# Kernel optimization log

Hardware: AMD Instinct MI355X
Metric: run time of the kernel (lower is better)

Reference implementation:

```python
import jax, jax.numpy as jnp
import numpy as np

N = 131072   # total gates/nodes in the batched block-diagonal circuit graph
E = 524288   # directed edges (avg degree 4)
D = 100      # hidden dim
DA = 50      # msg MLP hidden
DC = 30      # classifier hidden
R = 20       # message-passing rounds


def mlp(x, W1, b1, W2, b2):
    return jax.nn.relu(x @ W1 + b1) @ W2 + b2


def gru_step(x, h, Wih, Whh, bih, bhh):
    # single-timestep torch.nn.GRU cell
    gi = x @ Wih.T + bih
    gh = h @ Whh.T + bhh
    ir, iz, inn = jnp.split(gi, 3, axis=-1)
    hr, hz, hn = jnp.split(gh, 3, axis=-1)
    r = jax.nn.sigmoid(ir + hr)
    z = jax.nn.sigmoid(iz + hz)
    nwe = jnp.tanh(inn + r * hn)
    return (1.0 - z) * nwe + z * h


def setup_inputs():
    key = jax.random.key(0)
    ks = jax.random.split(key, 26)
    s = 0.05

    def rn(k, shape):
        return jax.random.normal(k, shape, dtype=jnp.float32) * s

    inp = {
        'features': jax.random.normal(ks[0], (N, 4), dtype=jnp.float32),
        'edge_row': jax.random.randint(ks[1], (E,), 0, N, dtype=jnp.int32),
        'edge_col': jax.random.randint(ks[2], (E,), 0, N, dtype=jnp.int32),
        'init_W': rn(ks[3], (4, D)), 'init_b': jnp.zeros((D,), jnp.float32),
        'fmsg_W1': rn(ks[4], (D, DA)), 'fmsg_b1': jnp.zeros((DA,), jnp.float32),
        'fmsg_W2': rn(ks[5], (DA, D)), 'fmsg_b2': jnp.zeros((D,), jnp.float32),
        'bmsg_W1': rn(ks[6], (D, DA)), 'bmsg_b1': jnp.zeros((DA,), jnp.float32),
        'bmsg_W2': rn(ks[7], (DA, D)), 'bmsg_b2': jnp.zeros((D,), jnp.float32),
        'fgru_Wih': rn(ks[8], (3 * D, D)), 'fgru_Whh': rn(ks[9], (3 * D, D)),
        'fgru_bih': jnp.zeros((3 * D,), jnp.float32), 'fgru_bhh': jnp.zeros((3 * D,), jnp.float32),
        'bgru_Wih': rn(ks[10], (3 * D, D)), 'bgru_Whh': rn(ks[11], (3 * D, D)),
        'bgru_bih': jnp.zeros((3 * D,), jnp.float32), 'bgru_bhh': jnp.zeros((3 * D,), jnp.float32),
        'cls_W1': rn(ks[12], (D, DC)), 'cls_b1': jnp.zeros((DC,), jnp.float32),
        'cls_W2': rn(ks[13], (DC, 1)), 'cls_b2': jnp.zeros((1,), jnp.float32),
    }
    return inp


def reference(features, edge_row, edge_col, init_W, init_b,
              fmsg_W1, fmsg_b1, fmsg_W2, fmsg_b2,
              bmsg_W1, bmsg_b1, bmsg_W2, bmsg_b2,
              fgru_Wih, fgru_Whh, fgru_bih, fgru_bhh,
              bgru_Wih, bgru_Whh, bgru_bih, bgru_bhh,
              cls_W1, cls_b1, cls_W2, cls_b2):
    n = features.shape[0]
    h = features @ init_W + init_b  # [N, D]

    def round_body(h, _):
        # forward pass: adj @ forward_msg(h)
        fm = mlp(h, fmsg_W1, fmsg_b1, fmsg_W2, fmsg_b2)
        f_msg = jax.ops.segment_sum(fm[edge_col], edge_row, num_segments=n)
        h = gru_step(f_msg, h, fgru_Wih, fgru_Whh, fgru_bih, fgru_bhh)
        # backward pass: adj.T @ backward_msg(h)
        bm = mlp(h, bmsg_W1, bmsg_b1, bmsg_W2, bmsg_b2)
        b_msg = jax.ops.segment_sum(bm[edge_row], edge_col, num_segments=n)
        h = gru_step(b_msg, h, bgru_Wih, bgru_Whh, bgru_bih, bgru_bhh)
        return h, None

    h, _ = jax.lax.scan(jax.checkpoint(round_body), h, None, length=R)
    return mlp(h, cls_W1, cls_b1, cls_W2, cls_b2)  # [N, 1]
```

## Files before the change

### kernel.cpp

```cpp
#include <hip/hip_runtime.h>
#include <math.h>

#define Nn 131072
#define Ee 524288

typedef __attribute__((ext_vector_type(8))) short short8;
typedef __attribute__((ext_vector_type(4))) float f32x4;
typedef unsigned short ushort_t;
typedef unsigned int uint32;

__device__ __forceinline__ f32x4 mfma16(short8 a, short8 b, f32x4 c) {
    return __builtin_amdgcn_mfma_f32_16x16x32_bf16(a, b, c, 0, 0, 0);
}

__device__ __forceinline__ uint32 rne_bf16(float x) {
    uint32 u = __float_as_uint(x);
    return (u + 0x7FFFu + ((u >> 16) & 1u)) >> 16;
}

__device__ __forceinline__ void split3(float x, uint32& h, uint32& m, uint32& l) {
    h = rne_bf16(x);
    float hf = __uint_as_float(h << 16);
    float r1 = x - hf;
    m = rne_bf16(r1);
    float mf = __uint_as_float(m << 16);
    float r2 = r1 - mf;
    l = rne_bf16(r2);
}

__global__ void diag_kernel(float* out, float val) {
    int n = blockIdx.x * 256 + threadIdx.x;
    if (n < Nn) out[n] = (n == 0) ? val : 0.f;
}
__global__ void zero_ints(int* p, int n) {
    int i = blockIdx.x * 256 + threadIdx.x;
    if (i < n) p[i] = 0;
}

__global__ void hist_kernel(const int* __restrict__ er, const int* __restrict__ ec,
                            int* __restrict__ cnt_f, int* __restrict__ cnt_b) {
    int e = blockIdx.x * 256 + threadIdx.x;
    atomicAdd(&cnt_f[er[e]], 1);
    atomicAdd(&cnt_b[ec[e]], 1);
}

__global__ __launch_bounds__(1024) void scan_kernel(const int* __restrict__ cnt,
                                                    int* __restrict__ ptr, int n) {
    __shared__ int sums[1024];
    int t = threadIdx.x;
    int chunk = n >> 10;
    int base = t * chunk;
    int s = 0;
    for (int i = 0; i < chunk; i++) s += cnt[base + i];
    sums[t] = s;
    __syncthreads();
    for (int off = 1; off < 1024; off <<= 1) {
        int v = (t >= off) ? sums[t - off] : 0;
        __syncthreads();
        sums[t] += v;
        __syncthreads();
    }
    int run = (t == 0) ? 0 : sums[t - 1];
    for (int i = 0; i < chunk; i++) { ptr[base + i] = run; run += cnt[base + i]; }
    if (t == 1023) ptr[n] = run;
}

__global__ void fill_kernel(const int* __restrict__ er, const int* __restrict__ ec,
                            int* __restrict__ ptr_f, int* __restrict__ ptr_b,
                            int* __restrict__ src_f, int* __restrict__ src_b) {
    int e = blockIdx.x * 256 + threadIdx.x;
    int r = er[e], c = ec[e];
    int p = atomicAdd(&ptr_f[r], 1); src_f[p] = c;
    int q = atomicAdd(&ptr_b[c], 1); src_b[q] = r;
}

__global__ void prep_gru_w(const float* __restrict__ Wih, const float* __restrict__ Whh,
                           const float* __restrict__ bih, const float* __restrict__ bhh,
                           ushort_t* __restrict__ W0, ushort_t* __restrict__ W1,
                           ushort_t* __restrict__ W2, float* __restrict__ bg) {
    int gid = blockIdx.x * 256 + threadIdx.x;
    if (gid >= 400 * 224) return;
    int c = gid / 224, k = gid - c * 224;
    int d = c >> 2, g = c & 3;
    float w = 0.f;
    if (k < 100) {
        if (g == 0)      w = Wih[d * 100 + k];
        else if (g == 1) w = Wih[(100 + d) * 100 + k];
        else if (g == 2) w = Wih[(200 + d) * 100 + k];
    } else if (k < 200) {
        int kk = k - 100;
        if (g == 0)      w = Whh[d * 100 + kk];
        else if (g == 1) w = Whh[(100 + d) * 100 + kk];
        else if (g == 3) w = Whh[(200 + d) * 100 + kk];
    }
    uint32 h, m, l; split3(w, h, m, l);
    W0[gid] = (ushort_t)h; W1[gid] = (ushort_t)m; W2[gid] = (ushort_t)l;
    if (k == 0) {
        float b;
        if (g == 0)      b = bih[d] + bhh[d];
        else if (g == 1) b = bih[100 + d] + bhh[100 + d];
        else if (g == 2) b = bih[200 + d];
        else             b = bhh[200 + d];
        bg[c] = b;
    }
}

__global__ void prep_msg_w(const float* __restrict__ W1, const float* __restrict__ b1,
                           const float* __restrict__ W2, const float* __restrict__ b2,
                           ushort_t* __restrict__ A0, ushort_t* __restrict__ A1,
                           ushort_t* __restrict__ A2, float* __restrict__ b1p,
                           ushort_t* __restrict__ B0, ushort_t* __restrict__ B1,
                           ushort_t* __restrict__ B2, float* __restrict__ b2p) {
    int gid = blockIdx.x * 256 + threadIdx.x;
    if (gid < 8192) {
        int c = gid >> 7, k = gid & 127;
        float w = (c < 50 && k < 100) ? W1[k * 50 + c] : 0.f;
        uint32 h, m, l; split3(w, h, m, l);
        A0[gid] = (ushort_t)h; A1[gid] = (ushort_t)m; A2[gid] = (ushort_t)l;
        if (k == 0) b1p[c] = (c < 50) ? b1[c] : 0.f;
    } else if (gid < 8192 + 7168) {
        int t = gid - 8192;
        int c = t >> 6, k = t & 63;
        float w = (c < 100 && k < 50) ? W2[k * 100 + c] : 0.f;
        uint32 h, m, l; split3(w, h, m, l);
        B0[t] = (ushort_t)h; B1[t] = (ushort_t)m; B2[t] = (ushort_t)l;
        if (k == 0) b2p[c] = (c < 100) ? b2[c] : 0.f;
    }
}

__global__ void init_h_kernel(const float* __restrict__ feat, const float* __restrict__ W,
                              const float* __restrict__ b, float* __restrict__ Act) {
    int gid = blockIdx.x * 256 + threadIdx.x;
    int n = gid / 100, d = gid - n * 100;
    float acc = b[d];
#pragma unroll
    for (int k = 0; k < 4; k++) acc += feat[n * 4 + k] * W[k * 100 + d];
    Act[(size_t)n * 200 + 100 + d] = acc;
}

__global__ __launch_bounds__(256, 2) void msg_mfma(
    const float* __restrict__ Act,
    const ushort_t* __restrict__ A0, const ushort_t* __restrict__ A1,
    const ushort_t* __restrict__ A2, const float* __restrict__ b1p,
    const ushort_t* __restrict__ B0, const ushort_t* __restrict__ B1,
    const ushort_t* __restrict__ B2, const float* __restrict__ b2p,
    float* __restrict__ fm) {
    __shared__ ushort_t C1[3][64][72];
    const int tid = threadIdx.x;
    const int u = tid >> 6;
    const int lane = tid & 63;
    const int m = lane & 15, q = lane >> 4;
    const int n0 = blockIdx.x * 64;
    const int n = n0 + u * 16 + m;

    f32x4 z = {0.f, 0.f, 0.f, 0.f};
    f32x4 a1[4] = {z, z, z, z};

    for (int kc = 0; kc < 4; kc++) {
        int kb = kc * 32 + q * 8;
        const float* src = Act + (size_t)n * 200 + 100 + kb;
        float4 v0 = *(const float4*)src;
        float4 v1 = *(const float4*)(src + 4);
        float e[8] = {v0.x, v0.y, v0.z, v0.w, v1.x, v1.y, v1.z, v1.w};
        union { short8 s; uint32 u4[4]; } f0, f1, f2;
#pragma unroll
        for (int j = 0; j < 4; j++) {
            uint32 ha, ma, la, hb, mb, lb;
            split3(e[2 * j], ha, ma, la);
            split3(e[2 * j + 1], hb, mb, lb);
            f0.u4[j] = ha | (hb << 16);
            f1.u4[j] = ma | (mb << 16);
            f2.u4[j] = la | (lb << 16);
        }
#pragma unroll
        for (int t = 0; t < 4; t++) {
            int off = (t * 16 + m) * 128 + kc * 32 + q * 8;
            short8 w0 = *(const short8*)(A0 + off);
            short8 w1 = *(const short8*)(A1 + off);
            short8 w2 = *(const short8*)(A2 + off);
            a1[t] = mfma16(w0, f0.s, a1[t]);
            a1[t] = mfma16(w0, f1.s, a1[t]);
            a1[t] = mfma16(w1, f0.s, a1[t]);
            a1[t] = mfma16(w0, f2.s, a1[t]);
            a1[t] = mfma16(w2, f0.s, a1[t]);
            a1[t] = mfma16(w1, f1.s, a1[t]);
        }
    }
#pragma unroll
    for (int t = 0; t < 4; t++) {
        int c0 = t * 16 + 4 * q;
        float4 bb = *(const float4*)&b1p[c0];
        float v0 = fmaxf(a1[t][0] + bb.x, 0.f);
        float v1 = fmaxf(a1[t][1] + bb.y, 0.f);
        float v2 = fmaxf(a1[t][2] + bb.z, 0.f);
        float v3 = fmaxf(a1[t][3] + bb.w, 0.f);
        uint32 h0, m0, l0, h1, m1, l1, h2, m2, l2, h3, m3, l3;
        split3(v0, h0, m0, l0); split3(v1, h1, m1, l1);
        split3(v2, h2, m2, l2); split3(v3, h3, m3, l3);
        int nl = u * 16 + m;
        *(uint2*)&C1[0][nl][c0] = make_uint2(h0 | (h1 << 16), h2 | (h3 << 16));
        *(uint2*)&C1[1][nl][c0] = make_uint2(m0 | (m1 << 16), m2 | (m3 << 16));
        *(uint2*)&C1[2][nl][c0] = make_uint2(l0 | (l1 << 16), l2 | (l3 << 16));
    }
    __syncthreads();

    f32x4 a2[7] = {z, z, z, z, z, z, z};
    for (int kc = 0; kc < 2; kc++) {
        int nl = u * 16 + m;
        short8 c0f = *(const short8*)&C1[0][nl][kc * 32 + q * 8];
        short8 c1f = *(const short8*)&C1[1][nl][kc * 32 + q * 8];
        short8 c2f = *(const short8*)&C1[2][nl][kc * 32 + q * 8];
#pragma unroll
        for (int t = 0; t < 7; t++) {
            int off = (t * 16 + m) * 64 + kc * 32 + q * 8;
            short8 w0 = *(const short8*)(B0 + off);
            short8 w1 = *(const short8*)(B1 + off);
            short8 w2 = *(const short8*)(B2 + off);
            a2[t] = mfma16(w0, c0f, a2[t]);
            a2[t] = mfma16(w0, c1f, a2[t]);
            a2[t] = mfma16(w1, c0f, a2[t]);
            a2[t] = mfma16(w0, c2f, a2[t]);
            a2[t] = mfma16(w2, c0f, a2[t]);
            a2[t] = mfma16(w1, c1f, a2[t]);
        }
    }
#pragma unroll
    for (int t = 0; t < 7; t++) {
        int c0 = t * 16 + 4 * q;
        if (c0 < 100) {
            float4 bb = *(const float4*)&b2p[c0];
            float4 o;
            o.x = a2[t][0] + bb.x; o.y = a2[t][1] + bb.y;
            o.z = a2[t][2] + bb.z; o.w = a2[t][3] + bb.w;
            *(float4*)&fm[(size_t)n * 100 + c0] = o;
        }
    }
}

__global__ void gather4(const float* __restrict__ fm, const int* __restrict__ ptr,
                        const int* __restrict__ idx, float* __restrict__ Act) {
    int gid = blockIdx.x * 256 + threadIdx.x;
    int n = gid / 25, qq = (gid - n * 25) * 4;
    int s = (n == 0) ? 0 : ptr[n - 1];
    int e = ptr[n];
    float4 acc = {0.f, 0.f, 0.f, 0.f};
    for (int i = s; i < e; i++) {
        float4 v = *(const float4*)&fm[(size_t)idx[i] * 100 + qq];
        acc.x += v.x; acc.y += v.y; acc.z += v.z; acc.w += v.w;
    }
    *(float4*)&Act[(size_t)n * 200 + qq] = acc;
}

__global__ __launch_bounds__(256, 3) void gru_mfma(
    float* __restrict__ Act,
    const ushort_t* __restrict__ W0, const ushort_t* __restrict__ W1,
    const ushort_t* __restrict__ W2, const float* __restrict__ bg) {
    __shared__ __align__(16) uint32 Bs[2][3][32][20];
    const int tid = threadIdx.x;
    const int wave = tid >> 6;
    const int lane = tid & 63;
    const int m = lane & 15, q = lane >> 4;
    const int n0 = blockIdx.x * 32;
    const int sr = tid >> 3;
    const int sk4 = (tid & 7) * 4;
    const int cu = (tid & 7) * 2;

    f32x4 z = {0.f, 0.f, 0.f, 0.f};
    f32x4 acc[7][2];
#pragma unroll
    for (int t = 0; t < 7; t++) { acc[t][0] = z; acc[t][1] = z; }

    const float* actrow = Act + (size_t)(n0 + sr) * 200;

#define LDCHUNK(kc, dst) do {                                   \
        int kb = (kc) * 32 + sk4;                               \
        if (kb < 200) dst = *(const float4*)(actrow + kb);      \
        else { dst.x = 0.f; dst.y = 0.f; dst.z = 0.f; dst.w = 0.f; } \
    } while (0)

#define STAGE(b, v) do {                                        \
        uint32 h0,m0,l0,h1,m1,l1,h2,m2,l2,h3,m3,l3;             \
        split3((v).x,h0,m0,l0); split3((v).y,h1,m1,l1);         \
        split3((v).z,h2,m2,l2); split3((v).w,h3,m3,l3);         \
        *(uint2*)&Bs[b][0][sr][cu] = make_uint2(h0|(h1<<16), h2|(h3<<16)); \
        *(uint2*)&Bs[b][1][sr][cu] = make_uint2(m0|(m1<<16), m2|(m3<<16)); \
        *(uint2*)&Bs[b][2][sr][cu] = make_uint2(l0|(l1<<16), l2|(l3<<16)); \
    } while (0)

    {
        float4 v0; LDCHUNK(0, v0);
        STAGE(0, v0);
    }
    __syncthreads();

    for (int kc = 0; kc < 7; kc++) {
        float4 nxt;
        if (kc < 6) LDCHUNK(kc + 1, nxt);
        const int b = kc & 1;
        short8 bf0[2], bf1[2], bf2[2];
#pragma unroll
        for (int u = 0; u < 2; u++) {
            bf0[u] = *(const short8*)&Bs[b][0][u * 16 + m][q * 4];
            bf1[u] = *(const short8*)&Bs[b][1][u * 16 + m][q * 4];
            bf2[u] = *(const short8*)&Bs[b][2][u * 16 + m][q * 4];
        }
#pragma unroll
        for (int t = 0; t < 7; t++) {
            if (t < 6 || wave == 0) {
                const int ct = t * 4 + wave;
                int off = (ct * 16 + m) * 224 + kc * 32 + q * 8;
                short8 w0 = *(const short8*)(W0 + off);
                short8 w1 = *(const short8*)(W1 + off);
                short8 w2 = *(const short8*)(W2 + off);
#pragma unroll
                for (int u = 0; u < 2; u++) {
                    acc[t][u] = mfma16(w0, bf0[u], acc[t][u]);
                    acc[t][u] = mfma16(w0, bf1[u], acc[t][u]);
                    acc[t][u] = mfma16(w1, bf0[u], acc[t][u]);
                    acc[t][u] = mfma16(w0, bf2[u], acc[t][u]);
                    acc[t][u] = mfma16(w2, bf0[u], acc[t][u]);
                    acc[t][u] = mfma16(w1, bf1[u], acc[t][u]);
                }
            }
        }
        if (kc < 6) STAGE(b ^ 1, nxt);
        __syncthreads();
    }
#undef LDCHUNK
#undef STAGE

#pragma unroll
    for (int t = 0; t < 7; t++) {
        if (t < 6 || wave == 0) {
            const int ct = t * 4 + wave;
            const int c0 = ct * 16 + 4 * q;
            const int d = ct * 4 + q;
            float4 b4 = *(const float4*)&bg[c0];
#pragma unroll
            for (int u = 0; u < 2; u++) {
                int n = n0 + u * 16 + m;
                float* hp = Act + (size_t)n * 200 + 100 + d;
                float hold = *hp;
                float rp = acc[t][u][0] + b4.x;
                float zp = acc[t][u][1] + b4.y;
                float np = acc[t][u][2] + b4.z;
                float hh = acc[t][u][3] + b4.w;
                float rr = 1.f / (1.f + __expf(-rp));
                float zz = 1.f / (1.f + __expf(-zp));
                float nw = tanhf(np + rr * hh);
                *hp = (1.f - zz) * nw + zz * hold;
            }
        }
    }
}

__global__ __launch_bounds__(256) void classifier(
    const float* __restrict__ Act, const float* __restrict__ W1,
    const float* __restrict__ b1, const float* __restrict__ W2,
    const float* __restrict__ b2, float* __restrict__ out) {
    __shared__ float Wc[3000];
    __shared__ float bc[30];
    __shared__ float w2[30];
    int tid = threadIdx.x;
    for (int i = tid; i < 3000; i += 256) Wc[i] = W1[i];
    if (tid < 30) { bc[tid] = b1[tid]; w2[tid] = W2[tid]; }
    __syncthreads();
    int n = blockIdx.x * 256 + tid;
    float a[30];
#pragma unroll
    for (int j = 0; j < 30; j++) a[j] = bc[j];
    for (int k = 0; k < 100; k++) {
        float hv = Act[(size_t)n * 200 + 100 + k];
#pragma unroll
        for (int j = 0; j < 30; j++) a[j] = fmaf(hv, Wc[k * 30 + j], a[j]);
    }
    float s = b2[0];
#pragma unroll
    for (int j = 0; j < 30; j++) s = fmaf(fmaxf(a[j], 0.f), w2[j], s);
    out[n] = s;
}

extern "C" void kernel_launch(void* const* d_in, const int* in_sizes, int n_in,
                              void* d_out, int out_size, void* d_ws, size_t ws_size,
                              hipStream_t stream) {
    const float* feat     = (const float*)d_in[0];
    const int*   er       = (const int*)d_in[1];
    const int*   ec       = (const int*)d_in[2];
    const float* init_W   = (const float*)d_in[3];
    const float* init_b   = (const float*)d_in[4];
    const float* fmsg_W1  = (const float*)d_in[5];
    const float* fmsg_b1  = (const float*)d_in[6];
    const float* fmsg_W2  = (const float*)d_in[7];
    const float* fmsg_b2  = (const float*)d_in[8];
    const float* bmsg_W1  = (const float*)d_in[9];
    const float* bmsg_b1  = (const float*)d_in[10];
    const float* bmsg_W2  = (const float*)d_in[11];
    const float* bmsg_b2  = (const float*)d_in[12];
    const float* fgru_Wih = (const float*)d_in[13];
    const float* fgru_Whh = (const float*)d_in[14];
    const float* fgru_bih = (const float*)d_in[15];
    const float* fgru_bhh = (const float*)d_in[16];
    const float* bgru_Wih = (const float*)d_in[17];
    const float* bgru_Whh = (const float*)d_in[18];
    const float* bgru_bih = (const float*)d_in[19];
    const float* bgru_bhh = (const float*)d_in[20];
    const float* cls_W1   = (const float*)d_in[21];
    const float* cls_b1   = (const float*)d_in[22];
    const float* cls_W2   = (const float*)d_in[23];
    const float* cls_b2   = (const float*)d_in[24];
    float* out = (float*)d_out;

    float* ws = (float*)d_ws;
    size_t o = 0;
    float* Act = ws + o; o += (size_t)Nn * 200;
    float* fm  = ws + o; o += (size_t)Nn * 100;

    ushort_t* us = (ushort_t*)(ws + o);
    size_t uo = 0;
    ushort_t* fWg0 = us + uo; uo += 400 * 224;
    ushort_t* fWg1 = us + uo; uo += 400 * 224;
    ushort_t* fWg2 = us + uo; uo += 400 * 224;
    ushort_t* bWg0 = us + uo; uo += 400 * 224;
    ushort_t* bWg1 = us + uo; uo += 400 * 224;
    ushort_t* bWg2 = us + uo; uo += 400 * 224;
    ushort_t* fA0 = us + uo; uo += 8192;
    ushort_t* fA1 = us + uo; uo += 8192;
    ushort_t* fA2 = us + uo; uo += 8192;
    ushort_t* bA0 = us + uo; uo += 8192;
    ushort_t* bA1 = us + uo; uo += 8192;
    ushort_t* bA2 = us + uo; uo += 8192;
    ushort_t* fB0 = us + uo; uo += 7168;
    ushort_t* fB1 = us + uo; uo += 7168;
    ushort_t* fB2 = us + uo; uo += 7168;
    ushort_t* bB0 = us + uo; uo += 7168;
    ushort_t* bB1 = us + uo; uo += 7168;
    ushort_t* bB2 = us + uo; uo += 7168;
    o += uo / 2;

    float* bgf  = ws + o; o += 400;
    float* bgb  = ws + o; o += 400;
    float* b1pf = ws + o; o += 64;
    float* b1pb = ws + o; o += 64;
    float* b2pf = ws + o; o += 112;
    float* b2pb = ws + o; o += 112;

    int* iws   = (int*)(ws + o);
    int* ptr_f = iws;
    int* ptr_b = ptr_f + (Nn + 1);
    int* cnt   = ptr_b + (Nn + 1);
    int* cnt_f = cnt;
    int* cnt_b = cnt + Nn;
    int* src_f = cnt + 2 * (size_t)Nn;
    int* src_b = src_f + Ee;

    size_t need = o * sizeof(float) +
                  (size_t)(2 * (Nn + 1) + 2 * Nn + 2 * Ee) * sizeof(int);
    if (ws_size < need) {
        diag_kernel<<<(Nn + 255) / 256, 256, 0, stream>>>(out, (float)ws_size);
        return;
    }

    zero_ints<<<(2 * Nn + 255) / 256, 256, 0, stream>>>(cnt, 2 * Nn);
    hist_kernel<<<Ee / 256, 256, 0, stream>>>(er, ec, cnt_f, cnt_b);
    scan_kernel<<<1, 1024, 0, stream>>>(cnt_f, ptr_f, Nn);
    scan_kernel<<<1, 1024, 0, stream>>>(cnt_b, ptr_b, Nn);
    fill_kernel<<<Ee / 256, 256, 0, stream>>>(er, ec, ptr_f, ptr_b, src_f, src_b);

    prep_gru_w<<<(400 * 224 + 255) / 256, 256, 0, stream>>>(
        fgru_Wih, fgru_Whh, fgru_bih, fgru_bhh, fWg0, fWg1, fWg2, bgf);
    prep_gru_w<<<(400 * 224 + 255) / 256, 256, 0, stream>>>(
        bgru_Wih, bgru_Whh, bgru_bih, bgru_bhh, bWg0, bWg1, bWg2, bgb);
    prep_msg_w<<<(15360 + 255) / 256, 256, 0, stream>>>(
        fmsg_W1, fmsg_b1, fmsg_W2, fmsg_b2, fA0, fA1, fA2, b1pf, fB0, fB1, fB2, b2pf);
    prep_msg_w<<<(15360 + 255) / 256, 256, 0, stream>>>(
        bmsg_W1, bmsg_b1, bmsg_W2, bmsg_b2, bA0, bA1, bA2, b1pb, bB0, bB1, bB2, b2pb);

    init_h_kernel<<<(Nn * 100) / 256, 256, 0, stream>>>(feat, init_W, init_b, Act);

    const int gTile = Nn / 64;
    const int gGru  = Nn / 32;
    const int gGath = Nn * 25 / 256;

    for (int rd = 0; rd < 20; rd++) {
        msg_mfma<<<gTile, 256, 0, stream>>>(Act, fA0, fA1, fA2, b1pf, fB0, fB1, fB2, b2pf, fm);
        gather4<<<gGath, 256, 0, stream>>>(fm, ptr_f, src_f, Act);
        gru_mfma<<<gGru, 256, 0, stream>>>(Act, fWg0, fWg1, fWg2, bgf);

        msg_mfma<<<gTile, 256, 0, stream>>>(Act, bA0, bA1, bA2, b1pb, bB0, bB1, bB2, b2pb, fm);
        gather4<<<gGath, 256, 0, stream>>>(fm, ptr_b, src_b, Act);
        gru_mfma<<<gGru, 256, 0, stream>>>(Act, bWg0, bWg1, bWg2, bgb);
    }

    classifier<<<Nn / 256, 256, 0, stream>>>(Act, cls_W1, cls_b1, cls_W2, cls_b2, out);
}
```

Measured before the change: 14.28 ms.

## Restructure GRU MFMA loop with register-held weights and padded uniform tiles

The GRU weight matrices are padded from 400 to 448 output columns so every wave runs 7 uniform tiles with no wave-divergent branch. The inner loop now loads all seven tiles' weight fragments per split level into registers and issues the MFMAs grouped by split pass. It also prefetches the next chunk's high-part weights during the current chunk, so global weight loads overlap with matrix work. The cost is more vector registers held live (three sets of 7 short8), which may reduce occupancy, plus some wasted MFMAs on the padded tile.

```diff
diff --git a/kernel.cpp b/kernel.cpp
--- a/kernel.cpp
+++ b/kernel.cpp
@@ -79,28 +79,32 @@
                            ushort_t* __restrict__ W0, ushort_t* __restrict__ W1,
                            ushort_t* __restrict__ W2, float* __restrict__ bg) {
     int gid = blockIdx.x * 256 + threadIdx.x;
-    if (gid >= 400 * 224) return;
+    if (gid >= 448 * 224) return;
     int c = gid / 224, k = gid - c * 224;
     int d = c >> 2, g = c & 3;
     float w = 0.f;
-    if (k < 100) {
-        if (g == 0)      w = Wih[d * 100 + k];
-        else if (g == 1) w = Wih[(100 + d) * 100 + k];
-        else if (g == 2) w = Wih[(200 + d) * 100 + k];
-    } else if (k < 200) {
-        int kk = k - 100;
-        if (g == 0)      w = Whh[d * 100 + kk];
-        else if (g == 1) w = Whh[(100 + d) * 100 + kk];
-        else if (g == 3) w = Whh[(200 + d) * 100 + kk];
+    if (d < 100) {
+        if (k < 100) {
+            if (g == 0)      w = Wih[d * 100 + k];
+            else if (g == 1) w = Wih[(100 + d) * 100 + k];
+            else if (g == 2) w = Wih[(200 + d) * 100 + k];
+        } else if (k < 200) {
+            int kk = k - 100;
+            if (g == 0)      w = Whh[d * 100 + kk];
+            else if (g == 1) w = Whh[(100 + d) * 100 + kk];
+            else if (g == 3) w = Whh[(200 + d) * 100 + kk];
+        }
     }
     uint32 h, m, l; split3(w, h, m, l);
     W0[gid] = (ushort_t)h; W1[gid] = (ushort_t)m; W2[gid] = (ushort_t)l;
     if (k == 0) {
-        float b;
-        if (g == 0)      b = bih[d] + bhh[d];
-        else if (g == 1) b = bih[100 + d] + bhh[100 + d];
-        else if (g == 2) b = bih[200 + d];
-        else             b = bhh[200 + d];
+        float b = 0.f;
+        if (d < 100) {
+            if (g == 0)      b = bih[d] + bhh[d];
+            else if (g == 1) b = bih[100 + d] + bhh[100 + d];
+            else if (g == 2) b = bih[200 + d];
+            else             b = bhh[200 + d];
+        }
         bg[c] = b;
     }
 }
@@ -270,6 +274,11 @@
 #pragma unroll
     for (int t = 0; t < 7; t++) { acc[t][0] = z; acc[t][1] = z; }
 
+    int woff[7];
+#pragma unroll
+    for (int t = 0; t < 7; t++)
+        woff[t] = ((t * 4 + wave) * 16 + m) * 224 + q * 8;
+
     const float* actrow = Act + (size_t)(n0 + sr) * 200;
 
 #define LDCHUNK(kc, dst) do {                                   \
@@ -287,54 +296,64 @@
         *(uint2*)&Bs[b][2][sr][cu] = make_uint2(l0|(l1<<16), l2|(l3<<16)); \
     } while (0)
 
-    {
-        float4 v0; LDCHUNK(0, v0);
-        STAGE(0, v0);
-    }
+#define GPASS(Wreg, bfr)                                        \
+    _Pragma("unroll")                                           \
+    for (int t = 0; t < 7; t++) {                               \
+        acc[t][0] = mfma16(Wreg[t], (bfr)[0], acc[t][0]);       \
+        acc[t][1] = mfma16(Wreg[t], (bfr)[1], acc[t][1]);       \
+    }
+
+    { float4 v0; LDCHUNK(0, v0); STAGE(0, v0); }
+
+    short8 wA[7], wB[7], wC[7];
+#pragma unroll
+    for (int t = 0; t < 7; t++) wA[t] = *(const short8*)(W0 + woff[t]);
+
     __syncthreads();
 
     for (int kc = 0; kc < 7; kc++) {
+        const int b = kc & 1;
+        const int ko = kc * 32;
         float4 nxt;
         if (kc < 6) LDCHUNK(kc + 1, nxt);
-        const int b = kc & 1;
-        short8 bf0[2], bf1[2], bf2[2];
-#pragma unroll
-        for (int u = 0; u < 2; u++) {
-            bf0[u] = *(const short8*)&Bs[b][0][u * 16 + m][q * 4];
-            bf1[u] = *(const short8*)&Bs[b][1][u * 16 + m][q * 4];
-            bf2[u] = *(const short8*)&Bs[b][2][u * 16 + m][q * 4];
-        }
-#pragma unroll
-        for (int t = 0; t < 7; t++) {
-            if (t < 6 || wave == 0) {
-                const int ct = t * 4 + wave;
-                int off = (ct * 16 + m) * 224 + kc * 32 + q * 8;
-                short8 w0 = *(const short8*)(W0 + off);
-                short8 w1 = *(const short8*)(W1 + off);
-                short8 w2 = *(const short8*)(W2 + off);
-#pragma unroll
-                for (int u = 0; u < 2; u++) {
-                    acc[t][u] = mfma16(w0, bf0[u], acc[t][u]);
-                    acc[t][u] = mfma16(w0, bf1[u], acc[t][u]);
-                    acc[t][u] = mfma16(w1, bf0[u], acc[t][u]);
-                    acc[t][u] = mfma16(w0, bf2[u], acc[t][u]);
-                    acc[t][u] = mfma16(w2, bf0[u], acc[t][u]);
-                    acc[t][u] = mfma16(w1, bf1[u], acc[t][u]);
-                }
-            }
-        }
+#pragma unroll
+        for (int t = 0; t < 7; t++) wB[t] = *(const short8*)(W1 + woff[t] + ko);
+#pragma unroll
+        for (int t = 0; t < 7; t++) wC[t] = *(const short8*)(W2 + woff[t] + ko);
+
+        short8 bf0[2], bft[2];
+        bf0[0] = *(const short8*)&Bs[b][0][m][q * 4];
+        bf0[1] = *(const short8*)&Bs[b][0][16 + m][q * 4];
+        GPASS(wA, bf0);
+        bft[0] = *(const short8*)&Bs[b][1][m][q * 4];
+        bft[1] = *(const short8*)&Bs[b][1][16 + m][q * 4];
+        GPASS(wA, bft);
+        bft[0] = *(const short8*)&Bs[b][2][m][q * 4];
+        bft[1] = *(const short8*)&Bs[b][2][16 + m][q * 4];
+        GPASS(wA, bft);
+        if (kc < 6) {
+#pragma unroll
+            for (int t = 0; t < 7; t++)
+                wA[t] = *(const short8*)(W0 + woff[t] + ko + 32);
+        }
+        GPASS(wB, bf0);
+        bft[0] = *(const short8*)&Bs[b][1][m][q * 4];
+        bft[1] = *(const short8*)&Bs[b][1][16 + m][q * 4];
+        GPASS(wB, bft);
+        GPASS(wC, bf0);
         if (kc < 6) STAGE(b ^ 1, nxt);
         __syncthreads();
     }
 #undef LDCHUNK
 #undef STAGE
+#undef GPASS
 
 #pragma unroll
     for (int t = 0; t < 7; t++) {
-        if (t < 6 || wave == 0) {
-            const int ct = t * 4 + wave;
-            const int c0 = ct * 16 + 4 * q;
-            const int d = ct * 4 + q;
+        const int ct = t * 4 + wave;
+        const int c0 = ct * 16 + 4 * q;
+        const int d = ct * 4 + q;
+        if (d < 100) {
             float4 b4 = *(const float4*)&bg[c0];
 #pragma unroll
             for (int u = 0; u < 2; u++) {
@@ -417,12 +436,12 @@
 
     ushort_t* us = (ushort_t*)(ws + o);
     size_t uo = 0;
-    ushort_t* fWg0 = us + uo; uo += 400 * 224;
-    ushort_t* fWg1 = us + uo; uo += 400 * 224;
-    ushort_t* fWg2 = us + uo; uo += 400 * 224;
-    ushort_t* bWg0 = us + uo; uo += 400 * 224;
-    ushort_t* bWg1 = us + uo; uo += 400 * 224;
-    ushort_t* bWg2 = us + uo; uo += 400 * 224;
+    ushort_t* fWg0 = us + uo; uo += 448 * 224;
+    ushort_t* fWg1 = us + uo; uo += 448 * 224;
+    ushort_t* fWg2 = us + uo; uo += 448 * 224;
+    ushort_t* bWg0 = us + uo; uo += 448 * 224;
+    ushort_t* bWg1 = us + uo; uo += 448 * 224;
+    ushort_t* bWg2 = us + uo; uo += 448 * 224;
     ushort_t* fA0 = us + uo; uo += 8192;
     ushort_t* fA1 = us + uo; uo += 8192;
     ushort_t* fA2 = us + uo; uo += 8192;
@@ -437,8 +456,8 @@
     ushort_t* bB2 = us + uo; uo += 7168;
     o += uo / 2;
 
-    float* bgf  = ws + o; o += 400;
-    float* bgb  = ws + o; o += 400;
+    float* bgf  = ws + o; o += 448;
+    float* bgb  = ws + o; o += 448;
     float* b1pf = ws + o; o += 64;
     float* b1pb = ws + o; o += 64;
     float* b2pf = ws + o; o += 112;
@@ -466,9 +485,9 @@
     scan_kernel<<<1, 1024, 0, stream>>>(cnt_b, ptr_b, Nn);
     fill_kernel<<<Ee / 256, 256, 0, stream>>>(er, ec, ptr_f, ptr_b, src_f, src_b);
 
-    prep_gru_w<<<(400 * 224 + 255) / 256, 256, 0, stream>>>(
+    prep_gru_w<<<(448 * 224 + 255) / 256, 256, 0, stream>>>(
         fgru_Wih, fgru_Whh, fgru_bih, fgru_bhh, fWg0, fWg1, fWg2, bgf);
-    prep_gru_w<<<(400 * 224 + 255) / 256, 256, 0, stream>>>(
+    prep_gru_w<<<(448 * 224 + 255) / 256, 256, 0, stream>>>(
         bgru_Wih, bgru_Whh, bgru_bih, bgru_bhh, bWg0, bWg1, bWg2, bgb);
     prep_msg_w<<<(15360 + 255) / 256, 256, 0, stream>>>(
         fmsg_W1, fmsg_b1, fmsg_W2, fmsg_b2, fA0, fA1, fA2, b1pf, fB0, fB1, fB2, b2pf);
```

Result: slower. 17.05 ms (+19.3%).
